# Performance work log

Measured on AMD Instinct MI355X. Metric: run time of the kernel, lower is better.

## Reference

```python
import jax, jax.numpy as jnp
import numpy as np

EPS = 1e-8
TAU = 0.2
IOU_THR = 0.5
NEG = -1e9
N, C, H, D_FG, D_CLS = 8192, 1024, 256, 64, 128


def setup_inputs() -> dict:
    key = jax.random.key(0)
    ks = jax.random.split(key, 11)
    def lin(k, fan_in, fan_out):
        return jax.random.normal(k, (fan_in, fan_out), jnp.float32) / np.sqrt(fan_in)
    return {
        "roi_feats": jax.random.normal(ks[0], (N, C), jnp.float32),
        "labels": jax.random.randint(ks[1], (N,), 0, 21, jnp.int32).astype(jnp.int64),
        "ious": jax.random.uniform(ks[2], (N,), jnp.float32),
        "fg_w1": lin(ks[3], C, H), "fg_b1": jnp.zeros((H,), jnp.float32),
        "fg_w2": lin(ks[4], H, D_FG), "fg_b2": jnp.zeros((D_FG,), jnp.float32),
        "cls_w1": lin(ks[5], C, H), "cls_b1": jnp.zeros((H,), jnp.float32),
        "cls_w2": lin(ks[6], H, D_CLS), "cls_b2": jnp.zeros((D_CLS,), jnp.float32),
    }


def _project_normalize(x, w1, b1, w2, b2):
    h = jax.nn.relu(x @ w1 + b1)
    z = h @ w2 + b2
    norm = jnp.maximum(jnp.linalg.norm(z, axis=1, keepdims=True), EPS)
    return z / norm


def _forward(roi_feats, labels, ious, fg_w1, fg_b1, fg_w2, fg_b2, cls_w1, cls_b1, cls_w2, cls_b2):
    n = roi_feats.shape[0]
    z_fg = _project_normalize(roi_feats, fg_w1, fg_b1, fg_w2, fg_b2)
    z_cls = _project_normalize(roi_feats, cls_w1, cls_b1, cls_w2, cls_b2)

    ignore = labels == -1
    fg = (labels > 0) & ~ignore
    iou_weight = jnp.where(ious > IOU_THR, ious, 0.0)
    eye = jnp.eye(n, dtype=bool)

    # ---- fg/bg contrastive (bg_as_negatives_only=True) ----
    sim_fg = (z_fg @ z_fg.T) / TAU                       # [N,N]
    exp_sim = jnp.exp(sim_fg)
    denom = jnp.sum(exp_sim * (~eye).astype(jnp.float32), axis=1)
    pos = (fg & ~ignore)[None, :] & ~eye                 # positives: fg columns, no self
    n_pos = jnp.sum(pos, axis=1)
    numer = jnp.sum(exp_sim * pos.astype(jnp.float32), axis=1)
    # original computes den = denom + EPS then -log((numer+EPS)/(den+EPS))
    loss_i = -jnp.log((numer + EPS) / (denom + 2.0 * EPS))
    valid = (fg & ~ignore) & (n_pos > 0)
    w = iou_weight * valid.astype(jnp.float32)
    loss_fg_bg = jnp.sum(w * loss_i) / (jnp.sum(w) + EPS)

    # ---- class supervised contrastive ----
    sim_cls = (z_cls @ z_cls.T) / TAU
    sim_masked = jnp.where(eye, NEG, sim_cls)
    log_denom = jax.nn.logsumexp(sim_masked, axis=1)     # [N]
    log_p = jnp.where(eye, NEG, sim_cls - log_denom[:, None])
    # pos_mask keeps diagonal (as in original): same label, col not ignore, col label != 0
    posc = (labels[None, :] == labels[:, None]) & (~ignore)[None, :] & (labels[None, :] != 0)
    n_posc = jnp.sum(posc, axis=1).astype(jnp.float32)
    sum_log_p = jnp.sum(log_p * posc.astype(jnp.float32), axis=1)
    valid_c = (fg & ~ignore) & (n_posc > 0) & jnp.isfinite(log_denom)
    Lzi = jnp.where(valid_c, -sum_log_p / (n_posc + EPS), 0.0)
    wc = iou_weight * valid_c.astype(jnp.float32)
    loss_supcon = jnp.sum(wc * Lzi) / (jnp.sum(wc) + EPS)

    return jnp.stack([loss_fg_bg, loss_supcon])


def reference(roi_feats, labels, ious, fg_w1, fg_b1, fg_w2, fg_b2, cls_w1, cls_b1, cls_w2, cls_b2):
    return _forward(roi_feats, labels, ious, fg_w1, fg_b1, fg_w2, fg_b2, cls_w1, cls_b1, cls_w2, cls_b2)
```

## Files before the change

kernel.cpp:

```cpp
#include <hip/hip_runtime.h>


typedef __attribute__((ext_vector_type(8))) short bs8;
typedef __attribute__((ext_vector_type(4))) float f4;

#define MFMA_BF16(a, b, c) __builtin_amdgcn_mfma_f32_16x16x32_bf16((a), (b), (c), 0, 0, 0)

#if defined(__has_builtin)
#if __has_builtin(__builtin_amdgcn_exp2f)
#define EXP2F(x) __builtin_amdgcn_exp2f(x)
#endif
#endif
#ifndef EXP2F
#define EXP2F(x) exp2f(x)
#endif

#define K_LOG2E 7.2134752044448170f

__device__ __forceinline__ unsigned short f2bf(float f) {
  unsigned int u = __float_as_uint(f);
  u = (u + 0x7fffu + ((u >> 16) & 1u)) >> 16;
  return (unsigned short)u;
}
__device__ __forceinline__ float bf2f(unsigned short s) {
  return __uint_as_float(((unsigned int)s) << 16);
}

constexpr size_t O_W1T  = 0;
constexpr size_t O_W2TF = 1048576;
constexpr size_t O_W2TC = 1081344;
constexpr size_t O_H    = 1146880;
constexpr size_t O_ZF   = 9535488;
constexpr size_t O_ZC   = 10584064;
constexpr size_t O_SCLS = 12681216;
constexpr size_t O_ROWD = 12697600;
constexpr size_t O_ROWN = 12730368;
constexpr size_t O_ROWS = 12763136;
constexpr size_t O_SCAL = 12795904;
constexpr size_t O_HIST = 12795920;
constexpr size_t O_NFG  = 12796048;
constexpr int ZERO_WORDS = (int)((O_NFG + 4 - O_SCLS) / 4);

__global__ void __launch_bounds__(256) zero_kernel(float* __restrict__ p, int n) {
  int i = blockIdx.x * 256 + threadIdx.x;
  if (i < n) p[i] = 0.f;
}

__global__ void __launch_bounds__(256) transp_kernel(
    const float* __restrict__ fgw1, const float* __restrict__ clsw1,
    const float* __restrict__ fgw2, const float* __restrict__ clsw2,
    unsigned short* __restrict__ W1T, unsigned short* __restrict__ W2Tf,
    unsigned short* __restrict__ W2Tc) {
  __shared__ float tile[64][65];
  const int m = blockIdx.y;
  const float* src;
  unsigned short* dst;
  int R, C;
  if (m == 0)      { src = fgw1;  dst = W1T;              R = 1024; C = 256; }
  else if (m == 1) { src = clsw1; dst = W1T + 256 * 1024; R = 1024; C = 256; }
  else if (m == 2) { src = fgw2;  dst = W2Tf;             R = 256;  C = 64;  }
  else             { src = clsw2; dst = W2Tc;             R = 256;  C = 128; }
  const int cT = C >> 6;
  if (blockIdx.x >= (R >> 6) * cT) return;
  const int r0 = (blockIdx.x / cT) << 6, c0 = (blockIdx.x % cT) << 6;
  const int t = threadIdx.x;
  {
    const int rr = t >> 4, cc = (t & 15) << 2;
#pragma unroll
    for (int i = 0; i < 4; i++) {
      float4 v = *(const float4*)(src + (size_t)(r0 + rr + i * 16) * C + c0 + cc);
      tile[rr + i * 16][cc] = v.x; tile[rr + i * 16][cc + 1] = v.y;
      tile[rr + i * 16][cc + 2] = v.z; tile[rr + i * 16][cc + 3] = v.w;
    }
  }
  __syncthreads();
  {
    const int dr = t >> 2, dc = (t & 3) << 4;
    bs8 o0, o1;
#pragma unroll
    for (int j = 0; j < 8; j++) o0[j] = (short)f2bf(tile[dc + j][dr]);
#pragma unroll
    for (int j = 0; j < 8; j++) o1[j] = (short)f2bf(tile[dc + 8 + j][dr]);
    unsigned short* dp = dst + (size_t)(c0 + dr) * R + r0 + dc;
    *(bs8*)dp = o0;
    *(bs8*)(dp + 8) = o1;
  }
}

__global__ void __launch_bounds__(256) meta_kernel(const int* __restrict__ labels,
                                                   int* __restrict__ hist,
                                                   int* __restrict__ nfg) {
  __shared__ int sh[33];
  const int t = threadIdx.x;
  if (t < 33) sh[t] = 0;
  __syncthreads();
  int lab = labels[blockIdx.x * 256 + t];
  if (lab >= 0 && lab < 32) atomicAdd(&sh[lab], 1);
  if (lab > 0) atomicAdd(&sh[32], 1);
  __syncthreads();
  if (t < 32 && sh[t] > 0) atomicAdd(&hist[t], sh[t]);
  if (t == 32 && sh[32] > 0) atomicAdd(nfg, sh[32]);
}

__global__ void __launch_bounds__(256) gemm1_kernel(
    const float* __restrict__ X, const unsigned short* __restrict__ W1T,
    const float* __restrict__ b1f, const float* __restrict__ b1c,
    unsigned short* __restrict__ H) {
  __shared__ __align__(16) unsigned short lA[128 * 40];
  __shared__ __align__(16) unsigned short lB[64 * 40];
  const int t = threadIdx.x;
  const int w = t >> 6, lane = t & 63, ln = lane & 15, quad = lane >> 4;
  const int m0 = blockIdx.x * 128, n0 = blockIdx.y * 64;

  f4 acc[2][4];
#pragma unroll
  for (int rs = 0; rs < 2; rs++)
#pragma unroll
    for (int s = 0; s < 4; s++) acc[rs][s] = (f4){0.f, 0.f, 0.f, 0.f};

  for (int k0 = 0; k0 < 1024; k0 += 32) {
    __syncthreads();
#pragma unroll
    for (int i = 0; i < 2; i++) {
      int ch = t + i * 256;
      int r = ch >> 2, c = (ch & 3) * 8;
      const float* xp = X + (size_t)(m0 + r) * 1024 + k0 + c;
      float4 x0 = *(const float4*)xp;
      float4 x1 = *(const float4*)(xp + 4);
      bs8 av;
      av[0] = (short)f2bf(x0.x); av[1] = (short)f2bf(x0.y);
      av[2] = (short)f2bf(x0.z); av[3] = (short)f2bf(x0.w);
      av[4] = (short)f2bf(x1.x); av[5] = (short)f2bf(x1.y);
      av[6] = (short)f2bf(x1.z); av[7] = (short)f2bf(x1.w);
      *(bs8*)&lA[r * 40 + c] = av;
    }
    {
      int r = t >> 2, c = (t & 3) * 8;
      *(bs8*)&lB[r * 40 + c] = *(const bs8*)(W1T + (size_t)(n0 + r) * 1024 + k0 + c);
    }
    __syncthreads();
    bs8 af0 = *(const bs8*)&lA[(w * 32 + ln) * 40 + quad * 8];
    bs8 af1 = *(const bs8*)&lA[(w * 32 + 16 + ln) * 40 + quad * 8];
#pragma unroll
    for (int s = 0; s < 4; s++) {
      bs8 bf = *(const bs8*)&lB[(s * 16 + ln) * 40 + quad * 8];
      acc[0][s] = MFMA_BF16(af0, bf, acc[0][s]);
      acc[1][s] = MFMA_BF16(af1, bf, acc[1][s]);
    }
  }
#pragma unroll
  for (int s = 0; s < 4; s++) {
    int n = n0 + s * 16 + ln;
    float b = (n < 256) ? b1f[n] : b1c[n - 256];
#pragma unroll
    for (int rs = 0; rs < 2; rs++)
#pragma unroll
      for (int r = 0; r < 4; r++) {
        float v = fmaxf(acc[rs][s][r] + b, 0.f);
        H[(size_t)(m0 + w * 32 + rs * 16 + quad * 4 + r) * 512 + n] = f2bf(v);
      }
  }
}

__global__ void __launch_bounds__(256) gemm2_kernel(
    const unsigned short* __restrict__ H,
    const unsigned short* __restrict__ W2Tf, const unsigned short* __restrict__ W2Tc,
    const float* __restrict__ b2f, const float* __restrict__ b2c,
    unsigned short* __restrict__ Zf, unsigned short* __restrict__ Zc) {
  const int t = threadIdx.x;
  const int w = t >> 6, lane = t & 63, ln = lane & 15, quad = lane >> 4;
  const int rw = blockIdx.x * 32 + (w & 1) * 16;

  if (w < 2) {
    const unsigned short* hrow = H + (size_t)(rw + ln) * 512;
    f4 acc[4];
#pragma unroll
    for (int s = 0; s < 4; s++) acc[s] = (f4){0.f, 0.f, 0.f, 0.f};
#pragma unroll
    for (int ks = 0; ks < 8; ks++) {
      bs8 af = *(const bs8*)(hrow + ks * 32 + quad * 8);
#pragma unroll
      for (int s = 0; s < 4; s++) {
        bs8 bf = *(const bs8*)(W2Tf + (size_t)(s * 16 + ln) * 256 + ks * 32 + quad * 8);
        acc[s] = MFMA_BF16(af, bf, acc[s]);
      }
    }
    float ss[4] = {0.f, 0.f, 0.f, 0.f};
#pragma unroll
    for (int s = 0; s < 4; s++) {
      float b = b2f[s * 16 + ln];
#pragma unroll
      for (int r = 0; r < 4; r++) {
        acc[s][r] += b;
        ss[r] = fmaf(acc[s][r], acc[s][r], ss[r]);
      }
    }
#pragma unroll
    for (int r = 0; r < 4; r++) {
#pragma unroll
      for (int off = 1; off < 16; off <<= 1) ss[r] += __shfl_xor(ss[r], off, 64);
      float sc = 1.f / fmaxf(sqrtf(ss[r]), 1e-8f);
#pragma unroll
      for (int s = 0; s < 4; s++)
        Zf[(size_t)(rw + quad * 4 + r) * 64 + s * 16 + ln] = f2bf(acc[s][r] * sc);
    }
  } else {
    const unsigned short* hrow = H + (size_t)(rw + ln) * 512 + 256;
    f4 acc[8];
#pragma unroll
    for (int s = 0; s < 8; s++) acc[s] = (f4){0.f, 0.f, 0.f, 0.f};
#pragma unroll
    for (int ks = 0; ks < 8; ks++) {
      bs8 af = *(const bs8*)(hrow + ks * 32 + quad * 8);
#pragma unroll
      for (int s = 0; s < 8; s++) {
        bs8 bf = *(const bs8*)(W2Tc + (size_t)(s * 16 + ln) * 256 + ks * 32 + quad * 8);
        acc[s] = MFMA_BF16(af, bf, acc[s]);
      }
    }
    float ss[4] = {0.f, 0.f, 0.f, 0.f};
#pragma unroll
    for (int s = 0; s < 8; s++) {
      float b = b2c[s * 16 + ln];
#pragma unroll
      for (int r = 0; r < 4; r++) {
        acc[s][r] += b;
        ss[r] = fmaf(acc[s][r], acc[s][r], ss[r]);
      }
    }
#pragma unroll
    for (int r = 0; r < 4; r++) {
#pragma unroll
      for (int off = 1; off < 16; off <<= 1) ss[r] += __shfl_xor(ss[r], off, 64);
      float sc = 1.f / fmaxf(sqrtf(ss[r]), 1e-8f);
#pragma unroll
      for (int s = 0; s < 8; s++)
        Zc[(size_t)(rw + quad * 4 + r) * 128 + s * 16 + ln] = f2bf(acc[s][r] * sc);
    }
  }
}

__global__ void __launch_bounds__(128) scls_kernel(const unsigned short* __restrict__ Zc,
                                                   const int* __restrict__ labels,
                                                   float* __restrict__ Scls) {
  const int c = blockIdx.x + 1;
  const int t = threadIdx.x;
  const int r0 = blockIdx.y * 256;
  float acc = 0.f;
#pragma unroll 4
  for (int r = r0; r < r0 + 256; r++) {
    if (labels[r] == c) acc += bf2f(Zc[(size_t)r * 128 + t]);
  }
  atomicAdd(&Scls[c * 128 + t], acc);
}

__global__ void __launch_bounds__(256) sim_kernel(
    const unsigned short* __restrict__ Zf, const unsigned short* __restrict__ Zc,
    const int* __restrict__ labels,
    float* __restrict__ rowD, float* __restrict__ rowN, float* __restrict__ rowS) {
  __shared__ __align__(16) unsigned short sZf[64 * 72];
  __shared__ __align__(16) unsigned short sZc[64 * 136];
  __shared__ float sFg[64];
  const int t = threadIdx.x;
  const int w = t >> 6, lane = t & 63, ln = lane & 15, quad = lane >> 4;
  const int rbase = blockIdx.x * 128 + w * 32;

  bs8 afg[2][2], acl[2][4];
#pragma unroll
  for (int rs = 0; rs < 2; rs++) {
    const unsigned short* zf = Zf + (size_t)(rbase + rs * 16 + ln) * 64;
    const unsigned short* zc = Zc + (size_t)(rbase + rs * 16 + ln) * 128;
#pragma unroll
    for (int s = 0; s < 2; s++) afg[rs][s] = *(const bs8*)(zf + s * 32 + quad * 8);
#pragma unroll
    for (int s = 0; s < 4; s++) acl[rs][s] = *(const bs8*)(zc + s * 32 + quad * 8);
  }

  float dacc[2][4] = {}, nacc[2][4] = {}, sacc[2][4] = {};

  for (int ct = 0; ct < 8; ct++) {
    const int c0 = blockIdx.y * 512 + ct * 64;
    __syncthreads();
#pragma unroll
    for (int i = 0; i < 2; i++) {
      int ch = t + i * 256;
      int j = ch >> 3, c8 = (ch & 7) * 8;
      *(bs8*)&sZf[j * 72 + c8] = *(const bs8*)(Zf + (size_t)(c0 + j) * 64 + c8);
    }
#pragma unroll
    for (int i = 0; i < 4; i++) {
      int ch = t + i * 256;
      int j = ch >> 4, c8 = (ch & 15) * 8;
      *(bs8*)&sZc[j * 136 + c8] = *(const bs8*)(Zc + (size_t)(c0 + j) * 128 + c8);
    }
    if (t < 64) sFg[t] = (labels[c0 + t] > 0) ? 1.f : 0.f;
    __syncthreads();

#pragma unroll
    for (int s = 0; s < 4; s++) {
      const int lcol = s * 16 + ln;
      const float fgc = sFg[lcol];
      bs8 b0 = *(const bs8*)&sZf[lcol * 72 + quad * 8];
      bs8 b1 = *(const bs8*)&sZf[lcol * 72 + 32 + quad * 8];
#pragma unroll
      for (int rs = 0; rs < 2; rs++) {
        f4 c = {0.f, 0.f, 0.f, 0.f};
        c = MFMA_BF16(afg[rs][0], b0, c);
        c = MFMA_BF16(afg[rs][1], b1, c);
#pragma unroll
        for (int r = 0; r < 4; r++) {
          float e = EXP2F(c[r] * K_LOG2E);
          dacc[rs][r] += e;
          nacc[rs][r] = fmaf(fgc, e, nacc[rs][r]);
        }
      }
      bs8 bc0 = *(const bs8*)&sZc[lcol * 136 + quad * 8];
      bs8 bc1 = *(const bs8*)&sZc[lcol * 136 + 32 + quad * 8];
      bs8 bc2 = *(const bs8*)&sZc[lcol * 136 + 64 + quad * 8];
      bs8 bc3 = *(const bs8*)&sZc[lcol * 136 + 96 + quad * 8];
#pragma unroll
      for (int rs = 0; rs < 2; rs++) {
        f4 c = {0.f, 0.f, 0.f, 0.f};
        c = MFMA_BF16(acl[rs][0], bc0, c);
        c = MFMA_BF16(acl[rs][1], bc1, c);
        c = MFMA_BF16(acl[rs][2], bc2, c);
        c = MFMA_BF16(acl[rs][3], bc3, c);
#pragma unroll
        for (int r = 0; r < 4; r++) sacc[rs][r] += EXP2F(c[r] * K_LOG2E);
      }
    }
  }

#pragma unroll
  for (int rs = 0; rs < 2; rs++)
#pragma unroll
    for (int r = 0; r < 4; r++) {
      float d = dacc[rs][r], n = nacc[rs][r], s = sacc[rs][r];
#pragma unroll
      for (int off = 1; off < 16; off <<= 1) {
        d += __shfl_xor(d, off, 64);
        n += __shfl_xor(n, off, 64);
        s += __shfl_xor(s, off, 64);
      }
      if (ln == 0) {
        int row = rbase + rs * 16 + quad * 4 + r;
        atomicAdd(&rowD[row], d);
        atomicAdd(&rowN[row], n);
        atomicAdd(&rowS[row], s);
      }
    }
}

__global__ void __launch_bounds__(256) finalize_kernel(
    const unsigned short* __restrict__ Zf, const unsigned short* __restrict__ Zc,
    const int* __restrict__ labels, const float* __restrict__ ious,
    const float* __restrict__ rowD, const float* __restrict__ rowN,
    const float* __restrict__ rowS, const float* __restrict__ Scls,
    const int* __restrict__ hist, const int* __restrict__ nfg,
    float* __restrict__ scal) {
  __shared__ float red[4][4];
  const int t = threadIdx.x, w = t >> 6, lane = t & 63;
  float aw0 = 0.f, al0 = 0.f, aw1 = 0.f, al1 = 0.f;
  const int NFG = *nfg;
  for (int it = 0; it < 16; it++) {
    const int i = it * 512 + blockIdx.x * 4 + w;
    const int lab = labels[i];
    if (lab > 0 && lab < 32) {
      const float iou = ious[i];
      const float iw = (iou > 0.5f) ? iou : 0.f;
      float dot = 0.f, ssq = 0.f;
#pragma unroll
      for (int p = 0; p < 2; p++) {
        const int k = lane + p * 64;
        const float z = bf2f(Zc[(size_t)i * 128 + k]);
        dot = fmaf(z, Scls[lab * 128 + k], dot);
        ssq = fmaf(z, z, ssq);
      }
      float zf = bf2f(Zf[(size_t)i * 64 + lane]);
      float ssqf = zf * zf;
#pragma unroll
      for (int off = 1; off < 64; off <<= 1) {
        dot += __shfl_xor(dot, off, 64);
        ssq += __shfl_xor(ssq, off, 64);
        ssqf += __shfl_xor(ssqf, off, 64);
      }
      if (lane == 0) {
        const float ef = EXP2F(K_LOG2E * ssqf);
        if (NFG - 1 > 0) {
          const float D = rowD[i] - ef;
          const float Nn = rowN[i] - ef;
          const float loss = logf(D + 2e-8f) - logf(Nn + 1e-8f);
          aw0 += iw;
          al0 += iw * loss;
        }
        const int npc = hist[lab];
        if (npc > 0) {
          const float S = rowS[i] - EXP2F(K_LOG2E * ssq);
          const float logden = logf(S);
          const float slp = (dot - ssq) * 5.0f - (float)(npc - 1) * logden - 1e9f;
          aw1 += iw;
          al1 += iw * (-slp / ((float)npc + 1e-8f));
        }
      }
    }
  }
  if (lane == 0) { red[w][0] = aw0; red[w][1] = al0; red[w][2] = aw1; red[w][3] = al1; }
  __syncthreads();
  if (t < 4) atomicAdd(&scal[t], red[0][t] + red[1][t] + red[2][t] + red[3][t]);
}

__global__ void writeout_kernel(const float* __restrict__ scal, float* __restrict__ out) {
  if (threadIdx.x == 0) {
    out[0] = scal[1] / (scal[0] + 1e-8f);
    out[1] = scal[3] / (scal[2] + 1e-8f);
  }
}

extern "C" void kernel_launch(void* const* d_in, const int* in_sizes, int n_in,
                              void* d_out, int out_size, void* d_ws, size_t ws_size,
                              hipStream_t stream) {
  (void)in_sizes; (void)n_in; (void)out_size; (void)ws_size;
  const float* roi    = (const float*)d_in[0];
  const int*   labels = (const int*)d_in[1];
  const float* ious   = (const float*)d_in[2];
  const float* fgw1   = (const float*)d_in[3];
  const float* fgb1   = (const float*)d_in[4];
  const float* fgw2   = (const float*)d_in[5];
  const float* fgb2   = (const float*)d_in[6];
  const float* clsw1  = (const float*)d_in[7];
  const float* clsb1  = (const float*)d_in[8];
  const float* clsw2  = (const float*)d_in[9];
  const float* clsb2  = (const float*)d_in[10];

  char* ws = (char*)d_ws;
  unsigned short* W1T  = (unsigned short*)(ws + O_W1T);
  unsigned short* W2Tf = (unsigned short*)(ws + O_W2TF);
  unsigned short* W2Tc = (unsigned short*)(ws + O_W2TC);
  unsigned short* Hb   = (unsigned short*)(ws + O_H);
  unsigned short* Zf   = (unsigned short*)(ws + O_ZF);
  unsigned short* Zc   = (unsigned short*)(ws + O_ZC);
  float* Scls = (float*)(ws + O_SCLS);
  float* rowD = (float*)(ws + O_ROWD);
  float* rowN = (float*)(ws + O_ROWN);
  float* rowS = (float*)(ws + O_ROWS);
  float* scal = (float*)(ws + O_SCAL);
  int* hist = (int*)(ws + O_HIST);
  int* nfg  = (int*)(ws + O_NFG);
  float* out = (float*)d_out;

  hipLaunchKernelGGL(zero_kernel, dim3((ZERO_WORDS + 255) / 256), dim3(256), 0, stream,
                     (float*)(ws + O_SCLS), ZERO_WORDS);
  hipLaunchKernelGGL(transp_kernel, dim3(64, 4), dim3(256), 0, stream,
                     fgw1, clsw1, fgw2, clsw2, W1T, W2Tf, W2Tc);
  hipLaunchKernelGGL(meta_kernel, dim3(32), dim3(256), 0, stream, labels, hist, nfg);
  hipLaunchKernelGGL(gemm1_kernel, dim3(64, 8), dim3(256), 0, stream,
                     roi, W1T, fgb1, clsb1, Hb);
  hipLaunchKernelGGL(gemm2_kernel, dim3(256), dim3(256), 0, stream,
                     Hb, W2Tf, W2Tc, fgb2, clsb2, Zf, Zc);
  hipLaunchKernelGGL(scls_kernel, dim3(20, 32), dim3(128), 0, stream, Zc, labels, Scls);
  hipLaunchKernelGGL(sim_kernel, dim3(64, 16), dim3(256), 0, stream,
                     Zf, Zc, labels, rowD, rowN, rowS);
  hipLaunchKernelGGL(finalize_kernel, dim3(128), dim3(256), 0, stream,
                     Zf, Zc, labels, ious, rowD, rowN, rowS, Scls, hist, nfg, scal);
  hipLaunchKernelGGL(writeout_kernel, dim3(1), dim3(64), 0, stream, scal, out);
}
```

Before: 220.1 us.

## Fold exp scale into normalization, drop LDS staging in sim kernel, truncate bf16 packing

The similarity kernel no longer stages column tiles of Zf and Zc through shared memory with barriers. Each lane now loads its B fragments straight from global memory, relying on L1/L2 cache. The 1/tau·log2e scale is folded into the normalization via sqrt, which removes a multiply before every exp2, and the finalize step is adjusted to match. The fp32 to bf16 conversion of X now uses a byte-permute truncation instead of round-to-nearest. This costs some accuracy, and scaling before rounding to bf16 changes precision slightly.

```diff
diff --git a/kernel.cpp b/kernel.cpp
--- a/kernel.cpp
+++ b/kernel.cpp
@@ -15,7 +15,8 @@
 #define EXP2F(x) exp2f(x)
 #endif
 
-#define K_LOG2E 7.2134752044448170f
+#define SQRT_KL2E 2.6857914f
+#define LN2F      0.6931471805599453f
 
 __device__ __forceinline__ unsigned short f2bf(float f) {
   unsigned int u = __float_as_uint(f);
@@ -24,6 +25,9 @@
 }
 __device__ __forceinline__ float bf2f(unsigned short s) {
   return __uint_as_float(((unsigned int)s) << 16);
+}
+__device__ __forceinline__ unsigned int pk_trunc(float a, float b) {
+  return __builtin_amdgcn_perm(__float_as_uint(b), __float_as_uint(a), 0x07060302u);
 }
 
 constexpr size_t O_W1T  = 0;
@@ -127,12 +131,12 @@
       const float* xp = X + (size_t)(m0 + r) * 1024 + k0 + c;
       float4 x0 = *(const float4*)xp;
       float4 x1 = *(const float4*)(xp + 4);
-      bs8 av;
-      av[0] = (short)f2bf(x0.x); av[1] = (short)f2bf(x0.y);
-      av[2] = (short)f2bf(x0.z); av[3] = (short)f2bf(x0.w);
-      av[4] = (short)f2bf(x1.x); av[5] = (short)f2bf(x1.y);
-      av[6] = (short)f2bf(x1.z); av[7] = (short)f2bf(x1.w);
-      *(bs8*)&lA[r * 40 + c] = av;
+      uint4 pk;
+      pk.x = pk_trunc(x0.x, x0.y);
+      pk.y = pk_trunc(x0.z, x0.w);
+      pk.z = pk_trunc(x1.x, x1.y);
+      pk.w = pk_trunc(x1.z, x1.w);
+      *(uint4*)&lA[r * 40 + c] = pk;
     }
     {
       int r = t >> 2, c = (t & 3) * 8;
@@ -199,7 +203,7 @@
     for (int r = 0; r < 4; r++) {
 #pragma unroll
       for (int off = 1; off < 16; off <<= 1) ss[r] += __shfl_xor(ss[r], off, 64);
-      float sc = 1.f / fmaxf(sqrtf(ss[r]), 1e-8f);
+      float sc = SQRT_KL2E / fmaxf(sqrtf(ss[r]), 1e-8f);
 #pragma unroll
       for (int s = 0; s < 4; s++)
         Zf[(size_t)(rw + quad * 4 + r) * 64 + s * 16 + ln] = f2bf(acc[s][r] * sc);
@@ -232,7 +236,7 @@
     for (int r = 0; r < 4; r++) {
 #pragma unroll
       for (int off = 1; off < 16; off <<= 1) ss[r] += __shfl_xor(ss[r], off, 64);
-      float sc = 1.f / fmaxf(sqrtf(ss[r]), 1e-8f);
+      float sc = SQRT_KL2E / fmaxf(sqrtf(ss[r]), 1e-8f);
 #pragma unroll
       for (int s = 0; s < 8; s++)
         Zc[(size_t)(rw + quad * 4 + r) * 128 + s * 16 + ln] = f2bf(acc[s][r] * sc);
@@ -258,9 +262,6 @@
     const unsigned short* __restrict__ Zf, const unsigned short* __restrict__ Zc,
     const int* __restrict__ labels,
     float* __restrict__ rowD, float* __restrict__ rowN, float* __restrict__ rowS) {
-  __shared__ __align__(16) unsigned short sZf[64 * 72];
-  __shared__ __align__(16) unsigned short sZc[64 * 136];
-  __shared__ float sFg[64];
   const int t = threadIdx.x;
   const int w = t >> 6, lane = t & 63, ln = lane & 15, quad = lane >> 4;
   const int rbase = blockIdx.x * 128 + w * 32;
@@ -277,57 +278,38 @@
   }
 
   float dacc[2][4] = {}, nacc[2][4] = {}, sacc[2][4] = {};
-
-  for (int ct = 0; ct < 8; ct++) {
-    const int c0 = blockIdx.y * 512 + ct * 64;
-    __syncthreads();
-#pragma unroll
-    for (int i = 0; i < 2; i++) {
-      int ch = t + i * 256;
-      int j = ch >> 3, c8 = (ch & 7) * 8;
-      *(bs8*)&sZf[j * 72 + c8] = *(const bs8*)(Zf + (size_t)(c0 + j) * 64 + c8);
-    }
-#pragma unroll
-    for (int i = 0; i < 4; i++) {
-      int ch = t + i * 256;
-      int j = ch >> 4, c8 = (ch & 15) * 8;
-      *(bs8*)&sZc[j * 136 + c8] = *(const bs8*)(Zc + (size_t)(c0 + j) * 128 + c8);
-    }
-    if (t < 64) sFg[t] = (labels[c0 + t] > 0) ? 1.f : 0.f;
-    __syncthreads();
-
-#pragma unroll
-    for (int s = 0; s < 4; s++) {
-      const int lcol = s * 16 + ln;
-      const float fgc = sFg[lcol];
-      bs8 b0 = *(const bs8*)&sZf[lcol * 72 + quad * 8];
-      bs8 b1 = *(const bs8*)&sZf[lcol * 72 + 32 + quad * 8];
-#pragma unroll
-      for (int rs = 0; rs < 2; rs++) {
-        f4 c = {0.f, 0.f, 0.f, 0.f};
-        c = MFMA_BF16(afg[rs][0], b0, c);
-        c = MFMA_BF16(afg[rs][1], b1, c);
-#pragma unroll
-        for (int r = 0; r < 4; r++) {
-          float e = EXP2F(c[r] * K_LOG2E);
-          dacc[rs][r] += e;
-          nacc[rs][r] = fmaf(fgc, e, nacc[rs][r]);
-        }
-      }
-      bs8 bc0 = *(const bs8*)&sZc[lcol * 136 + quad * 8];
-      bs8 bc1 = *(const bs8*)&sZc[lcol * 136 + 32 + quad * 8];
-      bs8 bc2 = *(const bs8*)&sZc[lcol * 136 + 64 + quad * 8];
-      bs8 bc3 = *(const bs8*)&sZc[lcol * 136 + 96 + quad * 8];
-#pragma unroll
-      for (int rs = 0; rs < 2; rs++) {
-        f4 c = {0.f, 0.f, 0.f, 0.f};
-        c = MFMA_BF16(acl[rs][0], bc0, c);
-        c = MFMA_BF16(acl[rs][1], bc1, c);
-        c = MFMA_BF16(acl[rs][2], bc2, c);
-        c = MFMA_BF16(acl[rs][3], bc3, c);
-#pragma unroll
-        for (int r = 0; r < 4; r++) sacc[rs][r] += EXP2F(c[r] * K_LOG2E);
-      }
+  const int cbase = blockIdx.y * 512;
+
+#pragma unroll 2
+  for (int g = 0; g < 32; g++) {
+    const int col = cbase + g * 16 + ln;
+    const float fgc = (labels[col] > 0) ? 1.f : 0.f;
+    const unsigned short* zf = Zf + (size_t)col * 64 + quad * 8;
+    const unsigned short* zc = Zc + (size_t)col * 128 + quad * 8;
+    bs8 b0 = *(const bs8*)zf;
+    bs8 b1 = *(const bs8*)(zf + 32);
+    bs8 c0 = *(const bs8*)zc;
+    bs8 c1 = *(const bs8*)(zc + 32);
+    bs8 c2 = *(const bs8*)(zc + 64);
+    bs8 c3 = *(const bs8*)(zc + 96);
+#pragma unroll
+    for (int rs = 0; rs < 2; rs++) {
+      f4 cf = {0.f, 0.f, 0.f, 0.f};
+      cf = MFMA_BF16(afg[rs][0], b0, cf);
+      cf = MFMA_BF16(afg[rs][1], b1, cf);
+#pragma unroll
+      for (int r = 0; r < 4; r++) {
+        float e = EXP2F(cf[r]);
+        dacc[rs][r] += e;
+        nacc[rs][r] = fmaf(fgc, e, nacc[rs][r]);
+      }
+      f4 cs = {0.f, 0.f, 0.f, 0.f};
+      cs = MFMA_BF16(acl[rs][0], c0, cs);
+      cs = MFMA_BF16(acl[rs][1], c1, cs);
+      cs = MFMA_BF16(acl[rs][2], c2, cs);
+      cs = MFMA_BF16(acl[rs][3], c3, cs);
+#pragma unroll
+      for (int r = 0; r < 4; r++) sacc[rs][r] += EXP2F(cs[r]);
     }
   }
 
@@ -385,7 +367,7 @@
         ssqf += __shfl_xor(ssqf, off, 64);
       }
       if (lane == 0) {
-        const float ef = EXP2F(K_LOG2E * ssqf);
+        const float ef = EXP2F(ssqf);
         if (NFG - 1 > 0) {
           const float D = rowD[i] - ef;
           const float Nn = rowN[i] - ef;
@@ -395,9 +377,9 @@
         }
         const int npc = hist[lab];
         if (npc > 0) {
-          const float S = rowS[i] - EXP2F(K_LOG2E * ssq);
+          const float S = rowS[i] - EXP2F(ssq);
           const float logden = logf(S);
-          const float slp = (dot - ssq) * 5.0f - (float)(npc - 1) * logden - 1e9f;
+          const float slp = (dot - ssq) * LN2F - (float)(npc - 1) * logden - 1e9f;
           aw1 += iw;
           al1 += iw * (-slp / ((float)npc + 1e-8f));
         }
```

After: 271.2 us. 1.23x slower.
